# Performance work log

Measured on AMD Instinct MI355X. Metric: run time of the kernel, lower is better.

The kernel has to match this reference:

```python
import jax, jax.numpy as jnp
import numpy as np

B, T, D, H = 4, 2048, 1024, 16
HD = D // H  # 64


def setup_inputs() -> dict:
    key = jax.random.key(0)
    ks = jax.random.split(key, 9)
    s = 1.0 / np.sqrt(D)
    return {
        "x": jax.random.normal(ks[0], (B, T, D), dtype=jnp.float32),
        "Wq": jax.random.normal(ks[1], (D, D), dtype=jnp.float32) * s,
        "bq": jnp.zeros((D,), dtype=jnp.float32),
        "Wk": jax.random.normal(ks[2], (D, D), dtype=jnp.float32) * s,
        "bk": jnp.zeros((D,), dtype=jnp.float32),
        "Wv": jax.random.normal(ks[3], (D, D), dtype=jnp.float32) * s,
        "bv": jnp.zeros((D,), dtype=jnp.float32),
        "Wo": jax.random.normal(ks[4], (D, D), dtype=jnp.float32) * s,
        "bo": jnp.zeros((D,), dtype=jnp.float32),
    }


def reference(x, Wq, bq, Wk, bk, Wv, bv, Wo, bo):
    Bx, Tx, C = x.shape
    # QKV projections -> (B, H, T, HD)
    q = (x @ Wq + bq).reshape(Bx, Tx, H, HD).transpose(0, 2, 1, 3)
    k = (x @ Wk + bk).reshape(Bx, Tx, H, HD).transpose(0, 2, 1, 3)
    v = (x @ Wv + bv).reshape(Bx, Tx, H, HD).transpose(0, 2, 1, 3)
    # scaled dot-product scores (B, H, T, T)
    scores = jnp.einsum("bhqd,bhkd->bhqk", q, k) / jnp.sqrt(jnp.float32(HD))
    causal = jnp.tril(jnp.ones((Tx, Tx), dtype=bool))
    scores = jnp.where(causal[None, None, :, :], scores, jnp.float32(-1e9))
    attn = jax.nn.softmax(scores, axis=-1)
    out = jnp.einsum("bhqk,bhkd->bhqd", attn, v)  # (B, H, T, HD)
    out = out.transpose(0, 2, 1, 3).reshape(Bx, Tx, C)
    return out @ Wo + bo
```

## Files before the change

### kernel.cpp

```cpp
#include <hip/hip_runtime.h>


#define B_  4
#define T_  2048
#define D_  1024
#define H_  16
#define HD_ 64
#define M_  (B_ * T_)

typedef __bf16 bf16x8 __attribute__((ext_vector_type(8)));
typedef float  floatx4 __attribute__((ext_vector_type(4)));

__device__ __forceinline__ unsigned short f2b(float f) {
  unsigned int u = __float_as_uint(f);
  unsigned int r = (u + 0x7fffu + ((u >> 16) & 1u)) >> 16;
  return (unsigned short)r;
}

__device__ __forceinline__ float fast_exp2(float x) {
#if __has_builtin(__builtin_amdgcn_exp2f)
  return __builtin_amdgcn_exp2f(x);
#else
  return exp2f(x);
#endif
}

__device__ __forceinline__ void async_ld16(const void* g, void* l) {
  __builtin_amdgcn_global_load_lds(
      (const __attribute__((address_space(1))) void*)g,
      (__attribute__((address_space(3))) void*)l, 16, 0, 0);
}


__global__ void cast_fp32_to_bf16(const float* __restrict__ in,
                                  unsigned short* __restrict__ out, int n) {
  int i = (blockIdx.x * 256 + threadIdx.x) * 4;
  if (i >= n) return;
  float4 v = *(const float4*)(in + i);
  ushort4 o;
  o.x = f2b(v.x); o.y = f2b(v.y); o.z = f2b(v.z); o.w = f2b(v.w);
  *(ushort4*)(out + i) = o;
}

__global__ void transpose_cast(const float* __restrict__ W0, const float* __restrict__ W1,
                               const float* __restrict__ W2, const float* __restrict__ W3,
                               unsigned short* __restrict__ O0, unsigned short* __restrict__ O1,
                               unsigned short* __restrict__ O2, unsigned short* __restrict__ O3) {
  __shared__ float tile[32][33];
  int z = blockIdx.z;
  const float* W = z == 0 ? W0 : z == 1 ? W1 : z == 2 ? W2 : W3;
  unsigned short* O = z == 0 ? O0 : z == 1 ? O1 : z == 2 ? O2 : O3;
  int n0 = blockIdx.x * 32, k0 = blockIdx.y * 32;
  int tx = threadIdx.x, ty = threadIdx.y;
#pragma unroll
  for (int i = 0; i < 4; ++i)
    tile[ty + i * 8][tx] = W[(size_t)(k0 + ty + i * 8) * D_ + n0 + tx];
  __syncthreads();
#pragma unroll
  for (int i = 0; i < 4; ++i)
    O[(size_t)(n0 + ty + i * 8) * D_ + k0 + tx] = f2b(tile[tx][ty + i * 8]);
}


__global__ __launch_bounds__(256, 2)
void gemm_qkv(const unsigned short* __restrict__ A,
              const unsigned short* __restrict__ Wt,
              const float* __restrict__ bq, const float* __restrict__ bk,
              const float* __restrict__ bv,
              unsigned short* __restrict__ Qo, unsigned short* __restrict__ Ko,
              unsigned short* __restrict__ Vo) {
  __shared__ unsigned short As[128 * 32];
  __shared__ unsigned short Bs[128 * 32];
  const int K = D_;

  const int tid = threadIdx.x;
  const int wave = tid >> 6, lane = tid & 63;
  const int quad = lane >> 4, l16 = lane & 15;
  const int m0 = blockIdx.y * 128, n0 = blockIdx.x * 128;
  const int wm = (wave >> 1) * 64, wn = (wave & 1) * 64;

  const int c0 = wave * 2, c1 = c0 + 1;
  const int r0 = c0 * 16 + (lane >> 2);
  const int r1 = r0 + 16;
  const int kb = (lane & 3) * 8;

  const unsigned short* Ag0 = A + (size_t)(m0 + r0) * K + kb;
  const unsigned short* Ag1 = A + (size_t)(m0 + r1) * K + kb;
  const unsigned short* Bg0 = Wt + (size_t)(n0 + r0) * K + kb;
  const unsigned short* Bg1 = Wt + (size_t)(n0 + r1) * K + kb;

  floatx4 acc[4][4] = {};

  for (int kt = 0; kt < K; kt += 32) {
    async_ld16(Ag0 + kt, &As[c0 * 512]);
    async_ld16(Ag1 + kt, &As[c1 * 512]);
    async_ld16(Bg0 + kt, &Bs[c0 * 512]);
    async_ld16(Bg1 + kt, &Bs[c1 * 512]);
    __syncthreads();

    bf16x8 a[4], b[4];
#pragma unroll
    for (int i = 0; i < 4; ++i)
      a[i] = *(const bf16x8*)&As[(wm + i * 16 + l16) * 32 + quad * 8];
#pragma unroll
    for (int i = 0; i < 4; ++i)
      b[i] = *(const bf16x8*)&Bs[(wn + i * 16 + l16) * 32 + quad * 8];

#pragma unroll
    for (int mi = 0; mi < 4; ++mi)
#pragma unroll
      for (int ni = 0; ni < 4; ++ni)
        acc[mi][ni] = __builtin_amdgcn_mfma_f32_16x16x32_bf16(
            a[mi], b[ni], acc[mi][ni], 0, 0, 0);
    __syncthreads();
  }

  const int which = n0 >> 10;
  const float* bias = which == 0 ? bq : which == 1 ? bk : bv;
  unsigned short* Out = which == 0 ? Qo : which == 1 ? Ko : Vo;

#pragma unroll
  for (int mi = 0; mi < 4; ++mi) {
#pragma unroll
    for (int ni = 0; ni < 4; ++ni) {
#pragma unroll
      for (int r = 0; r < 4; ++r) {
        const int m = m0 + wm + mi * 16 + quad * 4 + r;
        const int n = n0 + wn + ni * 16 + l16;
        const float val = acc[mi][ni][r] + bias[n & 1023];
        const int b = m >> 11, t = m & (T_ - 1);
        const int nl = n & 1023;
        const int h = nl >> 6, d = nl & (HD_ - 1);
        size_t idx;
        if (which == 2) {
          const int tp = (t & ~63) | (((t & 15) << 2) | ((t >> 4) & 3));
          idx = ((size_t)(b * H_ + h) * HD_ + d) * T_ + tp;
        } else {
          idx = ((size_t)(b * H_ + h) * T_ + t) * HD_ + d;
        }
        Out[idx] = f2b(val);
      }
    }
  }
}


__global__ __launch_bounds__(256, 2)
void gemm_out(const unsigned short* __restrict__ A,
              const unsigned short* __restrict__ Bt,
              const float* __restrict__ bias,
              float* __restrict__ Cout, int N, int K) {
  __shared__ unsigned short As[128 * 32];
  __shared__ unsigned short Bs[128 * 32];

  const int tid = threadIdx.x;
  const int wave = tid >> 6, lane = tid & 63;
  const int quad = lane >> 4, l16 = lane & 15;
  const int m0 = blockIdx.y * 128, n0 = blockIdx.x * 128;
  const int wm = (wave >> 1) * 64, wn = (wave & 1) * 64;

  const int c0 = wave * 2, c1 = c0 + 1;
  const int r0 = c0 * 16 + (lane >> 2);
  const int r1 = r0 + 16;
  const int kb = (lane & 3) * 8;

  const unsigned short* Ag0 = A + (size_t)(m0 + r0) * K + kb;
  const unsigned short* Ag1 = A + (size_t)(m0 + r1) * K + kb;
  const unsigned short* Bg0 = Bt + (size_t)(n0 + r0) * K + kb;
  const unsigned short* Bg1 = Bt + (size_t)(n0 + r1) * K + kb;

  floatx4 acc[4][4] = {};

  for (int kt = 0; kt < K; kt += 32) {
    async_ld16(Ag0 + kt, &As[c0 * 512]);
    async_ld16(Ag1 + kt, &As[c1 * 512]);
    async_ld16(Bg0 + kt, &Bs[c0 * 512]);
    async_ld16(Bg1 + kt, &Bs[c1 * 512]);
    __syncthreads();

    bf16x8 a[4], b[4];
#pragma unroll
    for (int i = 0; i < 4; ++i)
      a[i] = *(const bf16x8*)&As[(wm + i * 16 + l16) * 32 + quad * 8];
#pragma unroll
    for (int i = 0; i < 4; ++i)
      b[i] = *(const bf16x8*)&Bs[(wn + i * 16 + l16) * 32 + quad * 8];

#pragma unroll
    for (int mi = 0; mi < 4; ++mi)
#pragma unroll
      for (int ni = 0; ni < 4; ++ni)
        acc[mi][ni] = __builtin_amdgcn_mfma_f32_16x16x32_bf16(
            a[mi], b[ni], acc[mi][ni], 0, 0, 0);
    __syncthreads();
  }

#pragma unroll
  for (int mi = 0; mi < 4; ++mi)
#pragma unroll
    for (int ni = 0; ni < 4; ++ni)
#pragma unroll
      for (int r = 0; r < 4; ++r) {
        const int m = m0 + wm + mi * 16 + quad * 4 + r;
        const int n = n0 + wn + ni * 16 + l16;
        Cout[(size_t)m * N + n] = acc[mi][ni][r] + bias[n];
      }
}


#define PSTR 72

template <bool MASKED>
__device__ __forceinline__ void attn_chunk(
    int kbse, int qw, int quad, int l16,
    const unsigned short* __restrict__ Ks,
    const unsigned short* __restrict__ Vs,
    const bf16x8 (&aq)[2][2], floatx4 (&o)[2][4], floatx4 (&lacc)[2],
    unsigned short* __restrict__ pl0, unsigned short* __restrict__ pl1,
    bf16x8 vones) {
  const int sw = l16 & 7;

  bf16x8 kf0[4], kf1[4];
#pragma unroll
  for (int j = 0; j < 4; ++j) {
    const unsigned short* kr = &Ks[(j * 16 + l16) * HD_];
    kf0[j] = *(const bf16x8*)&kr[(quad ^ sw) * 8];
    kf1[j] = *(const bf16x8*)&kr[((quad + 4) ^ sw) * 8];
  }

  floatx4 s[2][4] = {};
#pragma unroll
  for (int qt = 0; qt < 2; ++qt)
#pragma unroll
    for (int j = 0; j < 4; ++j) {
      s[qt][j] = __builtin_amdgcn_mfma_f32_16x16x32_bf16(aq[qt][0], kf0[j], s[qt][j], 0, 0, 0);
      s[qt][j] = __builtin_amdgcn_mfma_f32_16x16x32_bf16(aq[qt][1], kf1[j], s[qt][j], 0, 0, 0);
    }

  bf16x8 vf0[4], vf1[4];
#pragma unroll
  for (int d4 = 0; d4 < 4; ++d4) {
    const unsigned short* vr = &Vs[(d4 * 16 + l16) * 64];
    vf0[d4] = *(const bf16x8*)&vr[(quad ^ sw) * 8];
    vf1[d4] = *(const bf16x8*)&vr[((quad + 4) ^ sw) * 8];
  }

  const float SL = 0.125f * 1.44269504f;
  const float CB = 8.0f * 1.44269504f;
#pragma unroll
  for (int qt = 0; qt < 2; ++qt) {
    unsigned short* pw = qt ? pl1 : pl0;
#pragma unroll
    for (int r = 0; r < 4; ++r) {
      float v0 = s[qt][0][r], v1 = s[qt][1][r], v2 = s[qt][2][r], v3 = s[qt][3][r];
      if (MASKED) {
        const int qrow = qw + qt * 16 + quad * 4 + r;
        if (kbse + l16 > qrow)      v0 = -1e30f;
        if (kbse + 16 + l16 > qrow) v1 = -1e30f;
        if (kbse + 32 + l16 > qrow) v2 = -1e30f;
        if (kbse + 48 + l16 > qrow) v3 = -1e30f;
      }
      const float p0 = fast_exp2(__builtin_fmaf(v0, SL, -CB));
      const float p1 = fast_exp2(__builtin_fmaf(v1, SL, -CB));
      const float p2 = fast_exp2(__builtin_fmaf(v2, SL, -CB));
      const float p3 = fast_exp2(__builtin_fmaf(v3, SL, -CB));
      uint2 pk;
      pk.x = __builtin_amdgcn_perm(__float_as_uint(p1), __float_as_uint(p0), 0x07060302u);
      pk.y = __builtin_amdgcn_perm(__float_as_uint(p3), __float_as_uint(p2), 0x07060302u);
      *(uint2*)&pw[(quad * 4 + r) * PSTR + 4 * l16] = pk;
    }
  }

#pragma unroll
  for (int qt = 0; qt < 2; ++qt) {
    const unsigned short* pw = qt ? pl1 : pl0;
    const bf16x8 pf0 = *(const bf16x8*)&pw[l16 * PSTR + quad * 8];
    const bf16x8 pf1 = *(const bf16x8*)&pw[l16 * PSTR + 32 + quad * 8];
    lacc[qt] = __builtin_amdgcn_mfma_f32_16x16x32_bf16(pf0, vones, lacc[qt], 0, 0, 0);
    lacc[qt] = __builtin_amdgcn_mfma_f32_16x16x32_bf16(pf1, vones, lacc[qt], 0, 0, 0);
#pragma unroll
    for (int d4 = 0; d4 < 4; ++d4) {
      o[qt][d4] = __builtin_amdgcn_mfma_f32_16x16x32_bf16(pf0, vf0[d4], o[qt][d4], 0, 0, 0);
      o[qt][d4] = __builtin_amdgcn_mfma_f32_16x16x32_bf16(pf1, vf1[d4], o[qt][d4], 0, 0, 0);
    }
  }
}

__global__ __launch_bounds__(256, 2)
void attn_kernel(const unsigned short* __restrict__ Q,
                 const unsigned short* __restrict__ K,
                 const unsigned short* __restrict__ Vp,
                 unsigned short* __restrict__ O) {
  __shared__ __align__(16) unsigned short Ks[64 * HD_];
  __shared__ __align__(16) unsigned short Vs[HD_ * 64];
  __shared__ unsigned short Pl[4][2][16 * PSTR];

  const int bidx = blockIdx.x;
  const int xcd = bidx & 7;
  const int t = bidx >> 3;
  const int j = t >> 5;
  const int slot = t & 31;
  const int bh_local = slot >> 2;
  const int v = slot & 3;
  const int k4 = (j == 0) ? v : (j == 1) ? 15 - v : (j == 2) ? v + 4 : 11 - v;
  const int bh = (xcd << 3) | bh_local;

  const int wave = threadIdx.x >> 6, lane = threadIdx.x & 63;
  const int quad = lane >> 4, l16 = lane & 15;
  const int tile = k4 * 4 + wave;
  const int qw = tile * 32;

  const unsigned short* Qb = Q + (size_t)bh * T_ * HD_;
  const unsigned short* Kb = K + (size_t)bh * T_ * HD_;
  const unsigned short* Vb = Vp + (size_t)bh * HD_ * T_;

  bf16x8 aq[2][2];
#pragma unroll
  for (int qt = 0; qt < 2; ++qt) {
    const unsigned short* qp = Qb + (size_t)(qw + qt * 16 + l16) * HD_;
    aq[qt][0] = *(const bf16x8*)(qp + quad * 8);
    aq[qt][1] = *(const bf16x8*)(qp + 32 + quad * 8);
  }

  union { unsigned short u[8]; bf16x8 v8; } ones;
#pragma unroll
  for (int i = 0; i < 8; ++i) ones.u[i] = 0x3F80;

  floatx4 o[2][4] = {};
  floatx4 lacc[2] = {};

  const int rsub = lane >> 3;
  const int csw = ((lane & 7) ^ rsub) * 8;
  const int rA = 8 * wave;
  const int rB = 8 * (wave + 4);

  const int my_nfull = tile >> 1;
  const int nit = 2 * k4 + 2;

  for (int kc = 0; kc < nit; ++kc) {
    const int kbse = kc * 64;
    if (kc) __syncthreads();
    async_ld16(Kb + (size_t)(kbse + rA + rsub) * HD_ + csw, &Ks[rA * HD_]);
    async_ld16(Kb + (size_t)(kbse + rB + rsub) * HD_ + csw, &Ks[rB * HD_]);
    async_ld16(Vb + (size_t)(rA + rsub) * T_ + kbse + csw, &Vs[rA * 64]);
    async_ld16(Vb + (size_t)(rB + rsub) * T_ + kbse + csw, &Vs[rB * 64]);
    __syncthreads();

    if (kc < my_nfull)
      attn_chunk<false>(kbse, qw, quad, l16, Ks, Vs, aq, o, lacc,
                        &Pl[wave][0][0], &Pl[wave][1][0], ones.v8);
    else if (kc == my_nfull)
      attn_chunk<true>(kbse, qw, quad, l16, Ks, Vs, aq, o, lacc,
                       &Pl[wave][0][0], &Pl[wave][1][0], ones.v8);
  }

  const int b = bh >> 4, h = bh & 15;
#pragma unroll
  for (int qt = 0; qt < 2; ++qt) {
#pragma unroll
    for (int r = 0; r < 4; ++r) {
      const float inv = 1.0f / lacc[qt][r];
      const int tt = qw + qt * 16 + quad * 4 + r;
      unsigned short* orow = O + (size_t)(b * T_ + tt) * D_ + h * HD_;
      orow[l16]      = f2b(o[qt][0][r] * inv);
      orow[16 + l16] = f2b(o[qt][1][r] * inv);
      orow[32 + l16] = f2b(o[qt][2][r] * inv);
      orow[48 + l16] = f2b(o[qt][3][r] * inv);
    }
  }
}


extern "C" void kernel_launch(void* const* d_in, const int* in_sizes, int n_in,
                              void* d_out, int out_size, void* d_ws, size_t ws_size,
                              hipStream_t stream) {
  const float* x  = (const float*)d_in[0];
  const float* Wq = (const float*)d_in[1];
  const float* bq = (const float*)d_in[2];
  const float* Wk = (const float*)d_in[3];
  const float* bk = (const float*)d_in[4];
  const float* Wv = (const float*)d_in[5];
  const float* bv = (const float*)d_in[6];
  const float* Wo = (const float*)d_in[7];
  const float* bo = (const float*)d_in[8];
  float* out = (float*)d_out;

  char* ws = (char*)d_ws;
  const size_t MB = 1u << 20;
  unsigned short* xb  = (unsigned short*)(ws);
  unsigned short* Wqt = (unsigned short*)(ws + 16 * MB);
  unsigned short* Wkt = (unsigned short*)(ws + 18 * MB);
  unsigned short* Wvt = (unsigned short*)(ws + 20 * MB);
  unsigned short* Wot = (unsigned short*)(ws + 22 * MB);
  unsigned short* Qb  = (unsigned short*)(ws + 24 * MB);
  unsigned short* Kb  = (unsigned short*)(ws + 40 * MB);
  unsigned short* Vtb = (unsigned short*)(ws + 56 * MB);
  unsigned short* Ob  = xb;

  cast_fp32_to_bf16<<<dim3(M_ * D_ / 1024), dim3(256), 0, stream>>>(x, xb, M_ * D_);
  transpose_cast<<<dim3(32, 32, 4), dim3(32, 8), 0, stream>>>(
      Wq, Wk, Wv, Wo, Wqt, Wkt, Wvt, Wot);

  gemm_qkv<<<dim3(24, M_ / 128), dim3(256), 0, stream>>>(
      xb, Wqt, bq, bk, bv, Qb, Kb, Vtb);

  attn_kernel<<<dim3(1024), dim3(256), 0, stream>>>(Qb, Kb, Vtb, Ob);

  gemm_out<<<dim3(D_ / 128, M_ / 128), dim3(256), 0, stream>>>(
      Ob, Wot, bo, out, D_, D_);
}
```

Measured before the change: 268.5 us.

## Deepen GEMM K-tile to 64 and XOR-swizzle LDS layout in both projection GEMMs

Both the QKV and output projection GEMMs now stage 64-wide K slices per iteration instead of 32. This halves the number of barrier pairs per K loop and issues more async global-to-LDS loads per sync. The LDS tiles use an XOR swizzle of the 16-byte chunk index by row, so the MFMA fragment reads avoid bank conflicts. The cost is doubled LDS usage per block, which could affect occupancy at two blocks per CU.

```diff
diff --git a/kernel.cpp b/kernel.cpp
--- a/kernel.cpp
+++ b/kernel.cpp
@@ -69,8 +69,8 @@
               const float* __restrict__ bv,
               unsigned short* __restrict__ Qo, unsigned short* __restrict__ Ko,
               unsigned short* __restrict__ Vo) {
-  __shared__ unsigned short As[128 * 32];
-  __shared__ unsigned short Bs[128 * 32];
+  __shared__ __align__(16) unsigned short As[128 * 64];
+  __shared__ __align__(16) unsigned short Bs[128 * 64];
   const int K = D_;
 
   const int tid = threadIdx.x;
@@ -79,39 +79,43 @@
   const int m0 = blockIdx.y * 128, n0 = blockIdx.x * 128;
   const int wm = (wave >> 1) * 64, wn = (wave & 1) * 64;
 
-  const int c0 = wave * 2, c1 = c0 + 1;
-  const int r0 = c0 * 16 + (lane >> 2);
-  const int r1 = r0 + 16;
-  const int kb = (lane & 3) * 8;
-
-  const unsigned short* Ag0 = A + (size_t)(m0 + r0) * K + kb;
-  const unsigned short* Ag1 = A + (size_t)(m0 + r1) * K + kb;
-  const unsigned short* Bg0 = Wt + (size_t)(n0 + r0) * K + kb;
-  const unsigned short* Bg1 = Wt + (size_t)(n0 + r1) * K + kb;
+  const int rsub = lane >> 3;
+  const int csw = ((lane & 7) ^ rsub) * 8;
+  const int rw = wave * 32;
+
+  const unsigned short* Ag = A + (size_t)(m0 + rw + rsub) * K + csw;
+  const unsigned short* Bg = Wt + (size_t)(n0 + rw + rsub) * K + csw;
 
   floatx4 acc[4][4] = {};
 
-  for (int kt = 0; kt < K; kt += 32) {
-    async_ld16(Ag0 + kt, &As[c0 * 512]);
-    async_ld16(Ag1 + kt, &As[c1 * 512]);
-    async_ld16(Bg0 + kt, &Bs[c0 * 512]);
-    async_ld16(Bg1 + kt, &Bs[c1 * 512]);
+  for (int kt = 0; kt < K; kt += 64) {
+#pragma unroll
+    for (int j = 0; j < 4; ++j) {
+      async_ld16(Ag + (size_t)(j * 8) * K + kt, &As[(rw + j * 8) * 64]);
+      async_ld16(Bg + (size_t)(j * 8) * K + kt, &Bs[(rw + j * 8) * 64]);
+    }
     __syncthreads();
 
-    bf16x8 a[4], b[4];
-#pragma unroll
-    for (int i = 0; i < 4; ++i)
-      a[i] = *(const bf16x8*)&As[(wm + i * 16 + l16) * 32 + quad * 8];
-#pragma unroll
-    for (int i = 0; i < 4; ++i)
-      b[i] = *(const bf16x8*)&Bs[(wn + i * 16 + l16) * 32 + quad * 8];
-
-#pragma unroll
-    for (int mi = 0; mi < 4; ++mi)
-#pragma unroll
-      for (int ni = 0; ni < 4; ++ni)
-        acc[mi][ni] = __builtin_amdgcn_mfma_f32_16x16x32_bf16(
-            a[mi], b[ni], acc[mi][ni], 0, 0, 0);
+#pragma unroll
+    for (int kk = 0; kk < 2; ++kk) {
+      bf16x8 a[4], b[4];
+#pragma unroll
+      for (int i = 0; i < 4; ++i) {
+        const int ra = wm + i * 16 + l16;
+        a[i] = *(const bf16x8*)&As[ra * 64 + (((kk * 4 + quad) ^ (ra & 7)) * 8)];
+      }
+#pragma unroll
+      for (int i = 0; i < 4; ++i) {
+        const int rb = wn + i * 16 + l16;
+        b[i] = *(const bf16x8*)&Bs[rb * 64 + (((kk * 4 + quad) ^ (rb & 7)) * 8)];
+      }
+#pragma unroll
+      for (int mi = 0; mi < 4; ++mi)
+#pragma unroll
+        for (int ni = 0; ni < 4; ++ni)
+          acc[mi][ni] = __builtin_amdgcn_mfma_f32_16x16x32_bf16(
+              a[mi], b[ni], acc[mi][ni], 0, 0, 0);
+    }
     __syncthreads();
   }
 
@@ -150,8 +154,8 @@
               const unsigned short* __restrict__ Bt,
               const float* __restrict__ bias,
               float* __restrict__ Cout, int N, int K) {
-  __shared__ unsigned short As[128 * 32];
-  __shared__ unsigned short Bs[128 * 32];
+  __shared__ __align__(16) unsigned short As[128 * 64];
+  __shared__ __align__(16) unsigned short Bs[128 * 64];
 
   const int tid = threadIdx.x;
   const int wave = tid >> 6, lane = tid & 63;
@@ -159,39 +163,43 @@
   const int m0 = blockIdx.y * 128, n0 = blockIdx.x * 128;
   const int wm = (wave >> 1) * 64, wn = (wave & 1) * 64;
 
-  const int c0 = wave * 2, c1 = c0 + 1;
-  const int r0 = c0 * 16 + (lane >> 2);
-  const int r1 = r0 + 16;
-  const int kb = (lane & 3) * 8;
-
-  const unsigned short* Ag0 = A + (size_t)(m0 + r0) * K + kb;
-  const unsigned short* Ag1 = A + (size_t)(m0 + r1) * K + kb;
-  const unsigned short* Bg0 = Bt + (size_t)(n0 + r0) * K + kb;
-  const unsigned short* Bg1 = Bt + (size_t)(n0 + r1) * K + kb;
+  const int rsub = lane >> 3;
+  const int csw = ((lane & 7) ^ rsub) * 8;
+  const int rw = wave * 32;
+
+  const unsigned short* Ag = A + (size_t)(m0 + rw + rsub) * K + csw;
+  const unsigned short* Bg = Bt + (size_t)(n0 + rw + rsub) * K + csw;
 
   floatx4 acc[4][4] = {};
 
-  for (int kt = 0; kt < K; kt += 32) {
-    async_ld16(Ag0 + kt, &As[c0 * 512]);
-    async_ld16(Ag1 + kt, &As[c1 * 512]);
-    async_ld16(Bg0 + kt, &Bs[c0 * 512]);
-    async_ld16(Bg1 + kt, &Bs[c1 * 512]);
+  for (int kt = 0; kt < K; kt += 64) {
+#pragma unroll
+    for (int j = 0; j < 4; ++j) {
+      async_ld16(Ag + (size_t)(j * 8) * K + kt, &As[(rw + j * 8) * 64]);
+      async_ld16(Bg + (size_t)(j * 8) * K + kt, &Bs[(rw + j * 8) * 64]);
+    }
     __syncthreads();
 
-    bf16x8 a[4], b[4];
-#pragma unroll
-    for (int i = 0; i < 4; ++i)
-      a[i] = *(const bf16x8*)&As[(wm + i * 16 + l16) * 32 + quad * 8];
-#pragma unroll
-    for (int i = 0; i < 4; ++i)
-      b[i] = *(const bf16x8*)&Bs[(wn + i * 16 + l16) * 32 + quad * 8];
-
-#pragma unroll
-    for (int mi = 0; mi < 4; ++mi)
-#pragma unroll
-      for (int ni = 0; ni < 4; ++ni)
-        acc[mi][ni] = __builtin_amdgcn_mfma_f32_16x16x32_bf16(
-            a[mi], b[ni], acc[mi][ni], 0, 0, 0);
+#pragma unroll
+    for (int kk = 0; kk < 2; ++kk) {
+      bf16x8 a[4], b[4];
+#pragma unroll
+      for (int i = 0; i < 4; ++i) {
+        const int ra = wm + i * 16 + l16;
+        a[i] = *(const bf16x8*)&As[ra * 64 + (((kk * 4 + quad) ^ (ra & 7)) * 8)];
+      }
+#pragma unroll
+      for (int i = 0; i < 4; ++i) {
+        const int rb = wn + i * 16 + l16;
+        b[i] = *(const bf16x8*)&Bs[rb * 64 + (((kk * 4 + quad) ^ (rb & 7)) * 8)];
+      }
+#pragma unroll
+      for (int mi = 0; mi < 4; ++mi)
+#pragma unroll
+        for (int ni = 0; ni < 4; ++ni)
+          acc[mi][ni] = __builtin_amdgcn_mfma_f32_16x16x32_bf16(
+              a[mi], b[ni], acc[mi][ni], 0, 0, 0);
+    }
     __syncthreads();
   }
 
```

New measurement: 259.6 us. -3.3%, faster.
